# Performance work log

Measured on AMD Instinct MI355X. Metric: run time of the kernel, lower is better.

The kernel has to match this reference:

```python
import jax, jax.numpy as jnp
import numpy as np

L, H, C, T_BLOCK, V = 12, 12, 768, 1024, 50257
EPS = 1e-5


def setup_inputs() -> dict:
    key = jax.random.key(0)
    ks = jax.random.split(key, 16)
    s = 0.02
    inp = {
        "idx": jax.random.randint(ks[0], (4, 1024), 0, V),
        "wte": jax.random.normal(ks[1], (V, C), jnp.float32) * s,
        "wpe": jax.random.normal(ks[2], (T_BLOCK, C), jnp.float32) * s,
        "ln1_w": jnp.ones((L, C), jnp.float32),
        "ln1_b": jnp.zeros((L, C), jnp.float32),
        "w_qkv": jax.random.normal(ks[3], (L, C, 3 * C), jnp.float32) * s,
        "b_qkv": jnp.zeros((L, 3 * C), jnp.float32),
        "w_ao": jax.random.normal(ks[4], (L, C, C), jnp.float32) * s,
        "b_ao": jnp.zeros((L, C), jnp.float32),
        "ln2_w": jnp.ones((L, C), jnp.float32),
        "ln2_b": jnp.zeros((L, C), jnp.float32),
        "w_fc": jax.random.normal(ks[5], (L, C, 4 * C), jnp.float32) * s,
        "b_fc": jnp.zeros((L, 4 * C), jnp.float32),
        "w_fp": jax.random.normal(ks[6], (L, 4 * C, C), jnp.float32) * s,
        "b_fp": jnp.zeros((L, C), jnp.float32),
        "lnf_w": jnp.ones((C,), jnp.float32),
        "lnf_b": jnp.zeros((C,), jnp.float32),
        "w_head": jax.random.normal(ks[7], (C, 1), jnp.float32) * s,
    }
    return inp


def _ln(x, w, b):
    mu = jnp.mean(x, axis=-1, keepdims=True)
    var = jnp.var(x, axis=-1, keepdims=True)
    return (x - mu) * jax.lax.rsqrt(var + EPS) * w + b


def _gpt_forward(idx, wte, wpe, ln1_w, ln1_b, w_qkv, b_qkv, w_ao, b_ao,
                 ln2_w, ln2_b, w_fc, b_fc, w_fp, b_fp, lnf_w, lnf_b, w_head):
    B, T = idx.shape
    D = C // H  # head dim
    x = wte[idx] + wpe[:T]  # [B,T,C]
    causal = jnp.tril(jnp.ones((T, T), bool))  # [T,T]

    def block(x, p):
        l1w, l1b, wq, bq, wo, bo, l2w, l2b, wf, bf, wp, bp = p
        h = _ln(x, l1w, l1b)
        qkv = h @ wq + bq  # [B,T,3C]
        q, k, v = jnp.split(qkv, 3, axis=-1)
        q = q.reshape(B, T, H, D).transpose(0, 2, 1, 3)  # [B,H,T,D]
        k = k.reshape(B, T, H, D).transpose(0, 2, 1, 3)
        v = v.reshape(B, T, H, D).transpose(0, 2, 1, 3)
        att = jnp.einsum('bhqd,bhkd->bhqk', q, k) * (1.0 / np.sqrt(D))
        att = jnp.where(causal, att, -jnp.inf)
        att = jax.nn.softmax(att, axis=-1)
        y = jnp.einsum('bhqk,bhkd->bhqd', att, v)
        y = y.transpose(0, 2, 1, 3).reshape(B, T, C)
        x = x + (y @ wo + bo)
        h2 = _ln(x, l2w, l2b)
        x = x + (jax.nn.gelu(h2 @ wf + bf, approximate=True) @ wp + bp)
        return x, None

    layer_params = (ln1_w, ln1_b, w_qkv, b_qkv, w_ao, b_ao,
                    ln2_w, ln2_b, w_fc, b_fc, w_fp, b_fp)
    x, _ = jax.lax.scan(block, x, layer_params)
    x = _ln(x, lnf_w, lnf_b)
    return x @ w_head  # [B,T,1]


def reference(idx, wte, wpe, ln1_w, ln1_b, w_qkv, b_qkv, w_ao, b_ao,
              ln2_w, ln2_b, w_fc, b_fc, w_fp, b_fp, lnf_w, lnf_b, w_head):
    return _gpt_forward(idx, wte, wpe, ln1_w, ln1_b, w_qkv, b_qkv, w_ao, b_ao,
                        ln2_w, ln2_b, w_fc, b_fc, w_fp, b_fp, lnf_w, lnf_b, w_head)
```

## Files before the change

kernel.cpp:

```cpp
#include <hip/hip_runtime.h>


#define CN    768
#define NKV   2304
#define FCN   3072
#define TN    1024
#define BN    4
#define HN    12
#define NL    12
#define MTOT  4096

typedef __attribute__((ext_vector_type(4))) float f32x4;
typedef __attribute__((ext_vector_type(8))) short short8;

typedef const __attribute__((address_space(1))) void* gas_t;
typedef __attribute__((address_space(3))) void* las_t;

__device__ __forceinline__ unsigned short f2b(float f) {
    unsigned int u = __float_as_uint(f);
    u += 0x7fffu + ((u >> 16) & 1u);
    return (unsigned short)(u >> 16);
}
__device__ __forceinline__ float b2f(unsigned short h) {
    return __uint_as_float(((unsigned int)h) << 16);
}

__device__ __forceinline__ void gemm128(
        const unsigned short* __restrict__ A, int lda,
        const unsigned short* __restrict__ B, int ldb,
        int m0, int n0, int kbeg, int kend, f32x4 acc[4][4])
{
    __shared__ __align__(16) unsigned short As[128 * 32];
    __shared__ __align__(16) unsigned short Bs[128 * 32];
    const int tid  = threadIdx.x;
    const int wave = tid >> 6;
    const int lane = tid & 63;
    const int quad = lane >> 4;
    const int l16  = lane & 15;
    const int wm   = (wave & 1) * 64;
    const int wn   = (wave >> 1) * 64;
    const int srow = wave * 16 + (lane >> 2);
    const int scol = (lane & 3) << 3;
    const unsigned short* ag = A + (long)(m0 + srow) * lda + scol;
    const unsigned short* bg = B + (long)(n0 + srow) * ldb + scol;
    unsigned short* asw = As + wave * 512;
    unsigned short* bsw = Bs + wave * 512;

    for (int k0 = kbeg; k0 < kend; k0 += 32) {
        __syncthreads();
        __builtin_amdgcn_global_load_lds((gas_t)(ag + k0),                  (las_t)(asw),            16, 0, 0);
        __builtin_amdgcn_global_load_lds((gas_t)(ag + k0 + (long)64 * lda), (las_t)(asw + 64 * 32),  16, 0, 0);
        __builtin_amdgcn_global_load_lds((gas_t)(bg + k0),                  (las_t)(bsw),            16, 0, 0);
        __builtin_amdgcn_global_load_lds((gas_t)(bg + k0 + (long)64 * ldb), (las_t)(bsw + 64 * 32),  16, 0, 0);
        __syncthreads();
        short8 af[4], bf[4];
#pragma unroll
        for (int i = 0; i < 4; ++i)
            af[i] = *(const short8*)(As + (wm + i * 16 + l16) * 32 + quad * 8);
#pragma unroll
        for (int j = 0; j < 4; ++j)
            bf[j] = *(const short8*)(Bs + (wn + j * 16 + l16) * 32 + quad * 8);
#pragma unroll
        for (int i = 0; i < 4; ++i)
#pragma unroll
            for (int j = 0; j < 4; ++j)
                acc[i][j] = __builtin_amdgcn_mfma_f32_16x16x32_bf16(af[i], bf[j], acc[i][j], 0, 0, 0);
    }
}

__global__ __launch_bounds__(256) void k_qkv128(
        const unsigned short* __restrict__ A, const unsigned short* __restrict__ B,
        const float* __restrict__ bias,
        unsigned short* __restrict__ qb, unsigned short* __restrict__ kb,
        unsigned short* __restrict__ vt)
{
    f32x4 acc[4][4];
#pragma unroll
    for (int i = 0; i < 4; ++i)
#pragma unroll
        for (int j = 0; j < 4; ++j) acc[i][j] = 0.f;
    const int m0 = blockIdx.x * 128, n0 = blockIdx.y * 128;
    gemm128(A, CN, B, CN, m0, n0, 0, CN, acc);
    const int wave = threadIdx.x >> 6, lane = threadIdx.x & 63;
    const int quad = lane >> 4, l16 = lane & 15;
    const int wm = (wave & 1) * 64, wn = (wave >> 1) * 64;
#pragma unroll
    for (int j = 0; j < 4; ++j) {
        int col = n0 + wn + j * 16 + l16;
        float bv = bias[col];
        int which = col / CN;
        int cc = col - which * CN;
        int h = cc >> 6, d = cc & 63;
#pragma unroll
        for (int i = 0; i < 4; ++i) {
#pragma unroll
            for (int r = 0; r < 4; ++r) {
                int row = m0 + wm + i * 16 + quad * 4 + r;
                int b = row >> 10, t = row & 1023;
                int bh = b * HN + h;
                unsigned short val = f2b(acc[i][j][r] + bv);
                if (which == 0)      qb[(bh * TN + t) * 64 + d] = val;
                else if (which == 1) kb[(bh * TN + t) * 64 + d] = val;
                else                 vt[(bh * 64 + d) * TN + t] = val;
            }
        }
    }
}

__global__ __launch_bounds__(256) void k_fc128(
        const unsigned short* __restrict__ A, const unsigned short* __restrict__ B,
        const float* __restrict__ bias, unsigned short* __restrict__ G)
{
    f32x4 acc[4][4];
#pragma unroll
    for (int i = 0; i < 4; ++i)
#pragma unroll
        for (int j = 0; j < 4; ++j) acc[i][j] = 0.f;
    const int m0 = blockIdx.x * 128, n0 = blockIdx.y * 128;
    gemm128(A, CN, B, CN, m0, n0, 0, CN, acc);
    const int wave = threadIdx.x >> 6, lane = threadIdx.x & 63;
    const int quad = lane >> 4, l16 = lane & 15;
    const int wm = (wave & 1) * 64, wn = (wave >> 1) * 64;
#pragma unroll
    for (int j = 0; j < 4; ++j) {
        int col = n0 + wn + j * 16 + l16;
        float bv = bias[col];
#pragma unroll
        for (int i = 0; i < 4; ++i)
#pragma unroll
            for (int r = 0; r < 4; ++r) {
                int row = m0 + wm + i * 16 + quad * 4 + r;
                float u = acc[i][j][r] + bv;
                float c = 0.7978845608028654f * (u + 0.044715f * u * u * u);
                float g = 0.5f * u * (1.0f + tanhf(c));
                G[(long)row * FCN + col] = f2b(g);
            }
    }
}

__global__ __launch_bounds__(256) void k_res128(
        const unsigned short* __restrict__ A, int lda,
        const unsigned short* __restrict__ B, int K, int ksplit,
        const float* __restrict__ bias, float* __restrict__ X)
{
    f32x4 acc[4][4];
#pragma unroll
    for (int i = 0; i < 4; ++i)
#pragma unroll
        for (int j = 0; j < 4; ++j) acc[i][j] = 0.f;
    const int m0 = blockIdx.x * 128, n0 = blockIdx.y * 128;
    const int kz = blockIdx.z;
    const int klen = K / ksplit;
    gemm128(A, lda, B, K, m0, n0, kz * klen, kz * klen + klen, acc);
    const int wave = threadIdx.x >> 6, lane = threadIdx.x & 63;
    const int quad = lane >> 4, l16 = lane & 15;
    const int wm = (wave & 1) * 64, wn = (wave >> 1) * 64;
#pragma unroll
    for (int j = 0; j < 4; ++j) {
        int col = n0 + wn + j * 16 + l16;
        float bv = (kz == 0) ? bias[col] : 0.f;
#pragma unroll
        for (int i = 0; i < 4; ++i)
#pragma unroll
            for (int r = 0; r < 4; ++r) {
                int row = m0 + wm + i * 16 + quad * 4 + r;
                atomicAdd(&X[(long)row * CN + col], acc[i][j][r] + bv);
            }
    }
}

__global__ __launch_bounds__(256) void k_attn(
        const unsigned short* __restrict__ qb, const unsigned short* __restrict__ kb,
        const unsigned short* __restrict__ vt, unsigned short* __restrict__ y)
{
    __shared__ __align__(16) unsigned short Qs[128 * 64];
    __shared__ __align__(16) unsigned short Ks[64 * 64];
    __shared__ __align__(16) unsigned short Vs[64 * 64];
    __shared__ __align__(16) unsigned short Ps[4 * 32 * 70];

    const int tid  = threadIdx.x;
    const int wave = tid >> 6;
    const int lane = tid & 63;
    const int quad = lane >> 4;
    const int l16  = lane & 15;
    const int bm   = blockIdx.x;
    const int z    = blockIdx.z;

    const unsigned short* qg = qb + (long)z * TN * 64;
    const unsigned short* kg = kb + (long)z * TN * 64;
    const unsigned short* vg = vt + (long)z * 64 * TN;

    const int r8 = lane >> 3;
    const int sl = lane & 7;

#pragma unroll
    for (int c = 0; c < 4; ++c) {
        int chunk = wave * 4 + c;
        int row = chunk * 8 + r8;
        int slot = sl ^ (row & 7);
        __builtin_amdgcn_global_load_lds(
            (gas_t)(qg + (long)(bm * 128 + row) * 64 + slot * 8),
            (las_t)(Qs + chunk * 512), 16, 0, 0);
    }
    __syncthreads();

    short8 qf[2][2];
#pragma unroll
    for (int i = 0; i < 2; ++i)
#pragma unroll
        for (int ks = 0; ks < 2; ++ks) {
            int row = wave * 32 + i * 16 + l16;
            int slot = (ks * 4 + quad) ^ (row & 7);
            qf[i][ks] = *(const short8*)(Qs + row * 64 + slot * 8);
        }

    f32x4 acc[2][4];
#pragma unroll
    for (int i = 0; i < 2; ++i)
#pragma unroll
        for (int j = 0; j < 4; ++j) acc[i][j] = 0.f;
    float m_run[2][4], l_run[2][4];
#pragma unroll
    for (int i = 0; i < 2; ++i)
#pragma unroll
        for (int r = 0; r < 4; ++r) { m_run[i][r] = -3e38f; l_run[i][r] = 0.f; }

    const int qbase = bm * 128 + wave * 32;
    const int nt = 2 * bm + 2;
    unsigned short* pw = Ps + wave * (32 * 70);

    for (int t = 0; t < nt; ++t) {
        const int k0 = t * 64;
        __syncthreads();
#pragma unroll
        for (int c = 0; c < 2; ++c) {
            int chunk = wave * 2 + c;
            int row = chunk * 8 + r8;
            int slot = sl ^ (row & 7);
            __builtin_amdgcn_global_load_lds(
                (gas_t)(kg + (long)(k0 + row) * 64 + slot * 8),
                (las_t)(Ks + chunk * 512), 16, 0, 0);
            __builtin_amdgcn_global_load_lds(
                (gas_t)(vg + (long)row * TN + k0 + slot * 8),
                (las_t)(Vs + chunk * 512), 16, 0, 0);
        }
        __syncthreads();

        f32x4 s[2][4];
#pragma unroll
        for (int i = 0; i < 2; ++i)
#pragma unroll
            for (int j = 0; j < 4; ++j) s[i][j] = 0.f;
#pragma unroll
        for (int j = 0; j < 4; ++j) {
            int row = j * 16 + l16;
#pragma unroll
            for (int ks = 0; ks < 2; ++ks) {
                int slot = (ks * 4 + quad) ^ (row & 7);
                short8 kf = *(const short8*)(Ks + row * 64 + slot * 8);
#pragma unroll
                for (int i = 0; i < 2; ++i)
                    s[i][j] = __builtin_amdgcn_mfma_f32_16x16x32_bf16(qf[i][ks], kf, s[i][j], 0, 0, 0);
            }
        }

#pragma unroll
        for (int i = 0; i < 2; ++i) {
#pragma unroll
            for (int r = 0; r < 4; ++r) {
                const int qrow = qbase + i * 16 + quad * 4 + r;
                float mx = -3e38f;
#pragma unroll
                for (int j = 0; j < 4; ++j) {
                    float v = s[i][j][r] * 0.125f;
                    if (k0 + j * 16 + l16 > qrow) v = -3e38f;
                    s[i][j][r] = v;
                    mx = fmaxf(mx, v);
                }
#pragma unroll
                for (int o = 1; o < 16; o <<= 1) mx = fmaxf(mx, __shfl_xor(mx, o));
                const float mnew = fmaxf(m_run[i][r], mx);
                const float resc = __expf(m_run[i][r] - mnew);
                m_run[i][r] = mnew;
                float ls = 0.f;
#pragma unroll
                for (int j = 0; j < 4; ++j) {
                    float p = __expf(s[i][j][r] - mnew);
                    s[i][j][r] = p;
                    ls += p;
                }
#pragma unroll
                for (int o = 1; o < 16; o <<= 1) ls += __shfl_xor(ls, o);
                l_run[i][r] = l_run[i][r] * resc + ls;
#pragma unroll
                for (int j = 0; j < 4; ++j)
                    acc[i][j][r] *= resc;
            }
        }

#pragma unroll
        for (int i = 0; i < 2; ++i)
#pragma unroll
            for (int j = 0; j < 4; ++j)
#pragma unroll
                for (int r = 0; r < 4; ++r)
                    pw[(i * 16 + quad * 4 + r) * 70 + j * 16 + l16] = f2b(s[i][j][r]);
        __syncthreads();

        short8 pa[2][2];
#pragma unroll
        for (int i = 0; i < 2; ++i)
#pragma unroll
            for (int ks = 0; ks < 2; ++ks)
                pa[i][ks] = *(const short8*)(pw + (i * 16 + l16) * 70 + ks * 32 + quad * 8);

#pragma unroll
        for (int j = 0; j < 4; ++j) {
            int row = j * 16 + l16;
#pragma unroll
            for (int ks = 0; ks < 2; ++ks) {
                int slot = (ks * 4 + quad) ^ (row & 7);
                short8 vf = *(const short8*)(Vs + row * 64 + slot * 8);
#pragma unroll
                for (int i = 0; i < 2; ++i)
                    acc[i][j] = __builtin_amdgcn_mfma_f32_16x16x32_bf16(pa[i][ks], vf, acc[i][j], 0, 0, 0);
            }
        }
    }

    const int b = z / HN, h = z - b * HN;
    unsigned short* yb = y + (long)b * TN * CN + h * 64;
#pragma unroll
    for (int i = 0; i < 2; ++i)
#pragma unroll
        for (int r = 0; r < 4; ++r) {
            const float inv = 1.0f / l_run[i][r];
            const int row = qbase + i * 16 + quad * 4 + r;
#pragma unroll
            for (int j = 0; j < 4; ++j)
                yb[(long)row * CN + j * 16 + l16] = f2b(acc[i][j][r] * inv);
        }
}

__device__ __forceinline__ float blk_sum(float v, float* red) {
#pragma unroll
    for (int o = 32; o > 0; o >>= 1) v += __shfl_xor(v, o);
    if ((threadIdx.x & 63) == 0) red[threadIdx.x >> 6] = v;
    __syncthreads();
    v = red[0] + red[1] + red[2] + red[3];
    __syncthreads();
    return v;
}

__global__ __launch_bounds__(256) void k_ln(
        const float* __restrict__ X, const float* __restrict__ w,
        const float* __restrict__ b, unsigned short* __restrict__ O)
{
    __shared__ float red[4];
    const int row = blockIdx.x, tid = threadIdx.x;
    const float* xr = X + (long)row * CN;
    float v[3], s = 0.f, sq = 0.f;
#pragma unroll
    for (int i = 0; i < 3; ++i) {
        v[i] = xr[tid + i * 256];
        s += v[i]; sq += v[i] * v[i];
    }
    s  = blk_sum(s, red);
    sq = blk_sum(sq, red);
    const float mu = s * (1.0f / CN);
    const float var = sq * (1.0f / CN) - mu * mu;
    const float rstd = rsqrtf(var + 1e-5f);
    unsigned short* orow = O + (long)row * CN;
#pragma unroll
    for (int i = 0; i < 3; ++i) {
        int c = tid + i * 256;
        orow[c] = f2b((v[i] - mu) * rstd * w[c] + b[c]);
    }
}

__global__ __launch_bounds__(256) void k_final(
        const float* __restrict__ X, const float* __restrict__ w,
        const float* __restrict__ b, const float* __restrict__ wh,
        float* __restrict__ out)
{
    __shared__ float red[4];
    const int row = blockIdx.x, tid = threadIdx.x;
    const float* xr = X + (long)row * CN;
    float v[3], s = 0.f, sq = 0.f;
#pragma unroll
    for (int i = 0; i < 3; ++i) {
        v[i] = xr[tid + i * 256];
        s += v[i]; sq += v[i] * v[i];
    }
    s  = blk_sum(s, red);
    sq = blk_sum(sq, red);
    const float mu = s * (1.0f / CN);
    const float rstd = rsqrtf(sq * (1.0f / CN) - mu * mu + 1e-5f);
    float acc = 0.f;
#pragma unroll
    for (int i = 0; i < 3; ++i) {
        int c = tid + i * 256;
        acc += ((v[i] - mu) * rstd * w[c] + b[c]) * wh[c];
    }
    acc = blk_sum(acc, red);
    if (tid == 0) out[row] = acc;
}

__global__ __launch_bounds__(256) void k_embed(
        const int* __restrict__ idx, const float* __restrict__ wte,
        const float* __restrict__ wpe, float* __restrict__ X)
{
    long e = (long)blockIdx.x * 256 + threadIdx.x;
    int c = (int)(e % CN);
    int bt = (int)(e / CN);
    int t = bt & 1023;
    int tok = idx[bt];
    X[e] = wte[(long)tok * CN + c] + wpe[(long)t * CN + c];
}

__global__ __launch_bounds__(256) void k_transpose(
        const float* __restrict__ in, unsigned short* __restrict__ out, int K, int N)
{
    __shared__ float tile[32][33];
    const int z = blockIdx.z;
    in  += (long)z * K * N;
    out += (long)z * K * N;
    const int n0 = blockIdx.x * 32, k0 = blockIdx.y * 32;
    const int tx = threadIdx.x & 31, ty = threadIdx.x >> 5;
#pragma unroll
    for (int i = 0; i < 4; ++i)
        tile[ty + i * 8][tx] = in[(long)(k0 + ty + i * 8) * N + n0 + tx];
    __syncthreads();
#pragma unroll
    for (int i = 0; i < 4; ++i)
        out[(long)(n0 + ty + i * 8) * K + k0 + tx] = f2b(tile[tx][ty + i * 8]);
}

extern "C" void kernel_launch(void* const* d_in, const int* in_sizes, int n_in,
                              void* d_out, int out_size, void* d_ws, size_t ws_size,
                              hipStream_t stream)
{
    const int*   idx    = (const int*)  d_in[0];
    const float* wte    = (const float*)d_in[1];
    const float* wpe    = (const float*)d_in[2];
    const float* ln1_w  = (const float*)d_in[3];
    const float* ln1_b  = (const float*)d_in[4];
    const float* w_qkv  = (const float*)d_in[5];
    const float* b_qkv  = (const float*)d_in[6];
    const float* w_ao   = (const float*)d_in[7];
    const float* b_ao   = (const float*)d_in[8];
    const float* ln2_w  = (const float*)d_in[9];
    const float* ln2_b  = (const float*)d_in[10];
    const float* w_fc   = (const float*)d_in[11];
    const float* b_fc   = (const float*)d_in[12];
    const float* w_fp   = (const float*)d_in[13];
    const float* b_fp   = (const float*)d_in[14];
    const float* lnf_w  = (const float*)d_in[15];
    const float* lnf_b  = (const float*)d_in[16];
    const float* w_head = (const float*)d_in[17];
    float* out = (float*)d_out;

    char* ws = (char*)d_ws;
    unsigned short* wqkvT = (unsigned short*)(ws + 0L);
    unsigned short* waoT  = (unsigned short*)(ws + 42467328L);
    unsigned short* wfcT  = (unsigned short*)(ws + 56623104L);
    unsigned short* wfpT  = (unsigned short*)(ws + 113246208L);
    float*          x     = (float*)         (ws + 169869312L);
    unsigned short* hb    = (unsigned short*)(ws + 182452224L);
    unsigned short* qb    = (unsigned short*)(ws + 188743680L);
    unsigned short* kb    = (unsigned short*)(ws + 195035136L);
    unsigned short* vt    = (unsigned short*)(ws + 201326592L);
    unsigned short* y     = (unsigned short*)(ws + 308281344L);
    unsigned short* g     = (unsigned short*)(ws + 314572800L);

    hipLaunchKernelGGL(k_transpose, dim3(NKV / 32, CN / 32, NL), dim3(256), 0, stream,
                       w_qkv, wqkvT, CN, NKV);
    hipLaunchKernelGGL(k_transpose, dim3(CN / 32, CN / 32, NL), dim3(256), 0, stream,
                       w_ao, waoT, CN, CN);
    hipLaunchKernelGGL(k_transpose, dim3(FCN / 32, CN / 32, NL), dim3(256), 0, stream,
                       w_fc, wfcT, CN, FCN);
    hipLaunchKernelGGL(k_transpose, dim3(CN / 32, FCN / 32, NL), dim3(256), 0, stream,
                       w_fp, wfpT, FCN, CN);

    hipLaunchKernelGGL(k_embed, dim3(MTOT * CN / 256), dim3(256), 0, stream,
                       idx, wte, wpe, x);

    for (int l = 0; l < NL; ++l) {
        hipLaunchKernelGGL(k_ln, dim3(MTOT), dim3(256), 0, stream,
                           x, ln1_w + l * CN, ln1_b + l * CN, hb);
        hipLaunchKernelGGL(k_qkv128, dim3(MTOT / 128, NKV / 128), dim3(256), 0, stream,
                           hb, wqkvT + (long)l * NKV * CN, b_qkv + l * NKV, qb, kb, vt);
        hipLaunchKernelGGL(k_attn, dim3(TN / 128, 1, BN * HN), dim3(256), 0, stream,
                           qb, kb, vt, y);
        hipLaunchKernelGGL(k_res128, dim3(MTOT / 128, CN / 128, 2), dim3(256), 0, stream,
                           y, CN, waoT + (long)l * CN * CN, CN, 2, b_ao + l * CN, x);
        hipLaunchKernelGGL(k_ln, dim3(MTOT), dim3(256), 0, stream,
                           x, ln2_w + l * CN, ln2_b + l * CN, hb);
        hipLaunchKernelGGL(k_fc128, dim3(MTOT / 128, FCN / 128), dim3(256), 0, stream,
                           hb, wfcT + (long)l * FCN * CN, b_fc + l * FCN, g);
        hipLaunchKernelGGL(k_res128, dim3(MTOT / 128, CN / 128, 4), dim3(256), 0, stream,
                           g, FCN, wfpT + (long)l * FCN * CN, FCN, 4, b_fp + l * CN, x);
    }

    hipLaunchKernelGGL(k_final, dim3(MTOT), dim3(256), 0, stream,
                       x, lnf_w, lnf_b, w_head, out);
}
```

Before: 3.426 ms.

## Pair causal attention q-blocks per workgroup and vectorize LN/embed kernels

Attention workgroups now each process two query blocks (x and 7-x), so every block does a similar amount of causal work and the grid shrinks by half. LayerNorm and final-head kernels switch to one wave per row with float4 loads and wave-shuffle reductions, which removes the shared-memory block reductions and barriers. Embedding uses float4 loads and stores. The risk is fewer attention workgroups (192) to fill the GPU, and serialized work inside each workgroup.

```diff
diff --git a/kernel.cpp b/kernel.cpp
--- a/kernel.cpp
+++ b/kernel.cpp
@@ -12,6 +12,7 @@
 
 typedef __attribute__((ext_vector_type(4))) float f32x4;
 typedef __attribute__((ext_vector_type(8))) short short8;
+typedef __attribute__((ext_vector_type(4))) unsigned short u16x4;
 
 typedef const __attribute__((address_space(1))) void* gas_t;
 typedef __attribute__((address_space(3))) void* las_t;
@@ -169,29 +170,22 @@
     }
 }
 
-__global__ __launch_bounds__(256) void k_attn(
-        const unsigned short* __restrict__ qb, const unsigned short* __restrict__ kb,
-        const unsigned short* __restrict__ vt, unsigned short* __restrict__ y)
-{
-    __shared__ __align__(16) unsigned short Qs[128 * 64];
-    __shared__ __align__(16) unsigned short Ks[64 * 64];
-    __shared__ __align__(16) unsigned short Vs[64 * 64];
-    __shared__ __align__(16) unsigned short Ps[4 * 32 * 70];
-
+__device__ __forceinline__ void flash_qblock(
+        int bm,
+        const unsigned short* __restrict__ qg, const unsigned short* __restrict__ kg,
+        const unsigned short* __restrict__ vg, unsigned short* __restrict__ yb,
+        unsigned short* Qs, unsigned short* Ks, unsigned short* Vs,
+        unsigned short* Ps)
+{
     const int tid  = threadIdx.x;
     const int wave = tid >> 6;
     const int lane = tid & 63;
     const int quad = lane >> 4;
     const int l16  = lane & 15;
-    const int bm   = blockIdx.x;
-    const int z    = blockIdx.z;
-
-    const unsigned short* qg = qb + (long)z * TN * 64;
-    const unsigned short* kg = kb + (long)z * TN * 64;
-    const unsigned short* vg = vt + (long)z * 64 * TN;
-
     const int r8 = lane >> 3;
     const int sl = lane & 7;
+
+    __syncthreads();
 
 #pragma unroll
     for (int c = 0; c < 4; ++c) {
@@ -328,8 +322,6 @@
         }
     }
 
-    const int b = z / HN, h = z - b * HN;
-    unsigned short* yb = y + (long)b * TN * CN + h * 64;
 #pragma unroll
     for (int i = 0; i < 2; ++i)
 #pragma unroll
@@ -342,39 +334,56 @@
         }
 }
 
-__device__ __forceinline__ float blk_sum(float v, float* red) {
-#pragma unroll
-    for (int o = 32; o > 0; o >>= 1) v += __shfl_xor(v, o);
-    if ((threadIdx.x & 63) == 0) red[threadIdx.x >> 6] = v;
-    __syncthreads();
-    v = red[0] + red[1] + red[2] + red[3];
-    __syncthreads();
-    return v;
+__global__ __launch_bounds__(256) void k_attn(
+        const unsigned short* __restrict__ qb, const unsigned short* __restrict__ kb,
+        const unsigned short* __restrict__ vt, unsigned short* __restrict__ y)
+{
+    __shared__ __align__(16) unsigned short Qs[128 * 64];
+    __shared__ __align__(16) unsigned short Ks[64 * 64];
+    __shared__ __align__(16) unsigned short Vs[64 * 64];
+    __shared__ __align__(16) unsigned short Ps[4 * 32 * 70];
+
+    const int x = blockIdx.x;
+    const int z = blockIdx.z;
+    const unsigned short* qg = qb + (long)z * TN * 64;
+    const unsigned short* kg = kb + (long)z * TN * 64;
+    const unsigned short* vg = vt + (long)z * 64 * TN;
+    const int b = z / HN, h = z - b * HN;
+    unsigned short* yb = y + (long)b * TN * CN + h * 64;
+
+    flash_qblock(x,     qg, kg, vg, yb, Qs, Ks, Vs, Ps);
+    flash_qblock(7 - x, qg, kg, vg, yb, Qs, Ks, Vs, Ps);
 }
 
 __global__ __launch_bounds__(256) void k_ln(
         const float* __restrict__ X, const float* __restrict__ w,
         const float* __restrict__ b, unsigned short* __restrict__ O)
 {
-    __shared__ float red[4];
-    const int row = blockIdx.x, tid = threadIdx.x;
-    const float* xr = X + (long)row * CN;
-    float v[3], s = 0.f, sq = 0.f;
+    const int row  = blockIdx.x * 4 + (threadIdx.x >> 6);
+    const int lane = threadIdx.x & 63;
+    const f32x4* xr = (const f32x4*)(X + (long)row * CN);
+    const f32x4* wv = (const f32x4*)w;
+    const f32x4* bv = (const f32x4*)b;
+    f32x4 v[3];
+    float s = 0.f, sq = 0.f;
 #pragma unroll
     for (int i = 0; i < 3; ++i) {
-        v[i] = xr[tid + i * 256];
-        s += v[i]; sq += v[i] * v[i];
-    }
-    s  = blk_sum(s, red);
-    sq = blk_sum(sq, red);
+        v[i] = xr[i * 64 + lane];
+#pragma unroll
+        for (int c = 0; c < 4; ++c) { s += v[i][c]; sq += v[i][c] * v[i][c]; }
+    }
+#pragma unroll
+    for (int o = 32; o > 0; o >>= 1) { s += __shfl_xor(s, o); sq += __shfl_xor(sq, o); }
     const float mu = s * (1.0f / CN);
-    const float var = sq * (1.0f / CN) - mu * mu;
-    const float rstd = rsqrtf(var + 1e-5f);
-    unsigned short* orow = O + (long)row * CN;
+    const float rstd = rsqrtf(sq * (1.0f / CN) - mu * mu + 1e-5f);
+    u16x4* orow = (u16x4*)(O + (long)row * CN);
 #pragma unroll
     for (int i = 0; i < 3; ++i) {
-        int c = tid + i * 256;
-        orow[c] = f2b((v[i] - mu) * rstd * w[c] + b[c]);
+        f32x4 wc = wv[i * 64 + lane], bc = bv[i * 64 + lane];
+        u16x4 o4;
+#pragma unroll
+        for (int c = 0; c < 4; ++c) o4[c] = f2b((v[i][c] - mu) * rstd * wc[c] + bc[c]);
+        orow[i * 64 + lane] = o4;
     }
 }
 
@@ -383,39 +392,49 @@
         const float* __restrict__ b, const float* __restrict__ wh,
         float* __restrict__ out)
 {
-    __shared__ float red[4];
-    const int row = blockIdx.x, tid = threadIdx.x;
-    const float* xr = X + (long)row * CN;
-    float v[3], s = 0.f, sq = 0.f;
+    const int row  = blockIdx.x * 4 + (threadIdx.x >> 6);
+    const int lane = threadIdx.x & 63;
+    const f32x4* xr = (const f32x4*)(X + (long)row * CN);
+    const f32x4* wv = (const f32x4*)w;
+    const f32x4* bv = (const f32x4*)b;
+    const f32x4* hv = (const f32x4*)wh;
+    f32x4 v[3];
+    float s = 0.f, sq = 0.f;
 #pragma unroll
     for (int i = 0; i < 3; ++i) {
-        v[i] = xr[tid + i * 256];
-        s += v[i]; sq += v[i] * v[i];
-    }
-    s  = blk_sum(s, red);
-    sq = blk_sum(sq, red);
+        v[i] = xr[i * 64 + lane];
+#pragma unroll
+        for (int c = 0; c < 4; ++c) { s += v[i][c]; sq += v[i][c] * v[i][c]; }
+    }
+#pragma unroll
+    for (int o = 32; o > 0; o >>= 1) { s += __shfl_xor(s, o); sq += __shfl_xor(sq, o); }
     const float mu = s * (1.0f / CN);
     const float rstd = rsqrtf(sq * (1.0f / CN) - mu * mu + 1e-5f);
     float acc = 0.f;
 #pragma unroll
     for (int i = 0; i < 3; ++i) {
-        int c = tid + i * 256;
-        acc += ((v[i] - mu) * rstd * w[c] + b[c]) * wh[c];
-    }
-    acc = blk_sum(acc, red);
-    if (tid == 0) out[row] = acc;
+        f32x4 wc = wv[i * 64 + lane], bc = bv[i * 64 + lane], hc = hv[i * 64 + lane];
+#pragma unroll
+        for (int c = 0; c < 4; ++c)
+            acc += ((v[i][c] - mu) * rstd * wc[c] + bc[c]) * hc[c];
+    }
+#pragma unroll
+    for (int o = 32; o > 0; o >>= 1) acc += __shfl_xor(acc, o);
+    if (lane == 0) out[row] = acc;
 }
 
 __global__ __launch_bounds__(256) void k_embed(
         const int* __restrict__ idx, const float* __restrict__ wte,
         const float* __restrict__ wpe, float* __restrict__ X)
 {
-    long e = (long)blockIdx.x * 256 + threadIdx.x;
-    int c = (int)(e % CN);
-    int bt = (int)(e / CN);
+    long i4 = (long)blockIdx.x * 256 + threadIdx.x;
+    int c4 = (int)(i4 % (CN / 4));
+    int bt = (int)(i4 / (CN / 4));
     int t = bt & 1023;
     int tok = idx[bt];
-    X[e] = wte[(long)tok * CN + c] + wpe[(long)t * CN + c];
+    f32x4 a = *(const f32x4*)(wte + (long)tok * CN + c4 * 4);
+    f32x4 p = *(const f32x4*)(wpe + (long)t * CN + c4 * 4);
+    *(f32x4*)(X + (long)bt * CN + c4 * 4) = a + p;
 }
 
 __global__ __launch_bounds__(256) void k_transpose(
@@ -482,19 +501,19 @@
     hipLaunchKernelGGL(k_transpose, dim3(CN / 32, FCN / 32, NL), dim3(256), 0, stream,
                        w_fp, wfpT, FCN, CN);
 
-    hipLaunchKernelGGL(k_embed, dim3(MTOT * CN / 256), dim3(256), 0, stream,
+    hipLaunchKernelGGL(k_embed, dim3(MTOT * (CN / 4) / 256), dim3(256), 0, stream,
                        idx, wte, wpe, x);
 
     for (int l = 0; l < NL; ++l) {
-        hipLaunchKernelGGL(k_ln, dim3(MTOT), dim3(256), 0, stream,
+        hipLaunchKernelGGL(k_ln, dim3(MTOT / 4), dim3(256), 0, stream,
                            x, ln1_w + l * CN, ln1_b + l * CN, hb);
         hipLaunchKernelGGL(k_qkv128, dim3(MTOT / 128, NKV / 128), dim3(256), 0, stream,
                            hb, wqkvT + (long)l * NKV * CN, b_qkv + l * NKV, qb, kb, vt);
-        hipLaunchKernelGGL(k_attn, dim3(TN / 128, 1, BN * HN), dim3(256), 0, stream,
+        hipLaunchKernelGGL(k_attn, dim3(TN / 256, 1, BN * HN), dim3(256), 0, stream,
                            qb, kb, vt, y);
         hipLaunchKernelGGL(k_res128, dim3(MTOT / 128, CN / 128, 2), dim3(256), 0, stream,
                            y, CN, waoT + (long)l * CN * CN, CN, 2, b_ao + l * CN, x);
-        hipLaunchKernelGGL(k_ln, dim3(MTOT), dim3(256), 0, stream,
+        hipLaunchKernelGGL(k_ln, dim3(MTOT / 4), dim3(256), 0, stream,
                            x, ln2_w + l * CN, ln2_b + l * CN, hb);
         hipLaunchKernelGGL(k_fc128, dim3(MTOT / 128, FCN / 128), dim3(256), 0, stream,
                            hb, wfcT + (long)l * FCN * CN, b_fc + l * FCN, g);
@@ -502,6 +521,6 @@
                            g, FCN, wfpT + (long)l * FCN * CN, FCN, 4, b_fp + l * CN, x);
     }
 
-    hipLaunchKernelGGL(k_final, dim3(MTOT), dim3(256), 0, stream,
+    hipLaunchKernelGGL(k_final, dim3(MTOT / 4), dim3(256), 0, stream,
                        x, lnf_w, lnf_b, w_head, out);
 }
```

Result: faster. 3.239 ms (-5.4%).
